# Kernel optimization log

Hardware: AMD Instinct MI355X
Metric: run time of the kernel (lower is better)

## Reference

```python
import jax, jax.numpy as jnp
import numpy as np

SCALING = 2.0  # lora alpha / r

def setup_inputs() -> dict:
    key = jax.random.key(0)
    k1, k2, k3, k4, k5 = jax.random.split(key, 5)
    B, S, D_IN, D_OUT, R = 4, 2048, 4096, 4096, 16
    x = jax.random.normal(k1, (B, S, D_IN), dtype=jnp.float32)
    weight = jax.random.normal(k2, (D_OUT, D_IN), dtype=jnp.float32) * 0.02
    lora_A = jax.random.normal(k3, (R, D_IN), dtype=jnp.float32) * (1.0 / np.sqrt(D_IN))
    lora_B = jax.random.normal(k4, (D_OUT, R), dtype=jnp.float32) * 0.02
    bias = jax.random.normal(k5, (D_OUT,), dtype=jnp.float32) * 0.02
    return {"x": x, "weight": weight, "lora_A": lora_A, "lora_B": lora_B, "bias": bias}

def reference(x, weight, lora_A, lora_B, bias):
    # Faithful to the torch module: materialize W + scaling * (B @ A), then F.linear.
    # effective_weight: [d_out, d_in]
    effective_weight = weight + SCALING * (lora_B @ lora_A)
    # F.linear(x, W, b) = x @ W.T + b
    out = jnp.einsum('bsd,od->bso', x, effective_weight) + bias
    return out
```

## Files before the change

### kernel.cpp

```cpp
#include <hip/hip_runtime.h>
#include <hip/hip_bf16.h>
#include <stdint.h>

typedef unsigned short u16;
typedef u16 u16x4 __attribute__((ext_vector_type(4)));
typedef short bf16x8 __attribute__((ext_vector_type(8)));
typedef float f32x4 __attribute__((ext_vector_type(4)));

__device__ __forceinline__ u16 f2bf(float f) {
  union { float f; uint32_t u; } v; v.f = f;
  uint32_t u = v.u;
  return (u16)((u + 0x7fffu + ((u >> 16) & 1u)) >> 16);
}

__global__ __launch_bounds__(256) void aux_kernel(
    const float4* __restrict__ x, u16x4* __restrict__ xb, int n4, int nW, int nCvt,
    const float* __restrict__ W, const float* __restrict__ A,
    const float* __restrict__ Bl, u16* __restrict__ Wout, int DIN) {
  if ((int)blockIdx.x < nW) {
    const int n0 = (int)blockIdx.x * 4;
    float bv[4][16];
#pragma unroll
    for (int j = 0; j < 4; ++j)
#pragma unroll
      for (int r = 0; r < 16; ++r) bv[j][r] = 2.0f * Bl[(n0 + j) * 16 + r];
    const int iters = DIN / (256 * 4);
    for (int c = 0; c < iters; ++c) {
      const int k = (c * 256 + (int)threadIdx.x) * 4;
      float4 wv[4];
#pragma unroll
      for (int j = 0; j < 4; ++j)
        wv[j] = *(const float4*)&W[(size_t)(n0 + j) * DIN + k];
#pragma unroll
      for (int r = 0; r < 16; ++r) {
        const float4 av = *(const float4*)&A[(size_t)r * DIN + k];
#pragma unroll
        for (int j = 0; j < 4; ++j) {
          wv[j].x += bv[j][r] * av.x;
          wv[j].y += bv[j][r] * av.y;
          wv[j].z += bv[j][r] * av.z;
          wv[j].w += bv[j][r] * av.w;
        }
      }
#pragma unroll
      for (int j = 0; j < 4; ++j) {
        u16x4 o;
        o.x = f2bf(wv[j].x); o.y = f2bf(wv[j].y);
        o.z = f2bf(wv[j].z); o.w = f2bf(wv[j].w);
        *(u16x4*)&Wout[(size_t)(n0 + j) * DIN + k] = o;
      }
    }
  } else {
    int i = ((int)blockIdx.x - nW) * 256 + threadIdx.x;
    const int stride = nCvt * 256;
    for (; i < n4; i += stride) {
      float4 v = x[i];
      u16x4 o;
      o.x = f2bf(v.x); o.y = f2bf(v.y); o.z = f2bf(v.z); o.w = f2bf(v.w);
      xb[i] = o;
    }
  }
}

#define BM 256
#define BN 256

__global__ __launch_bounds__(512, 2) void gemm256_kernel(
    const u16* __restrict__ A, const u16* __restrict__ B,
    const float* __restrict__ bias, float* __restrict__ C,
    int M, int N, int K) {
  extern __shared__ u16 lds[];

  const int tid  = threadIdx.x;
  const int lane = tid & 63;
  const int wid  = tid >> 6;

  const int nwg = gridDim.x;
  const int cpx = nwg >> 3;
  const int f   = ((int)blockIdx.x & 7) * cpx + ((int)blockIdx.x >> 3);
  const int nbx = N / BN;
  const int bx = f % nbx, by = f / nbx;
  const int bm = by * BM, bn = bx * BN;

  const int wmL = (wid >> 2) * 128;
  const int wnL = (wid & 3) * 64;
  const int lr  = lane & 15;
  const int lk  = lane >> 4;
  const int rslot = ((lk ^ ((lr >> 1) & 3)) << 3);

  const int srow  = tid >> 2;
  const int sslot = (((tid & 3) ^ ((tid >> 3) & 3)) << 3);
  const u16* gA = A + (size_t)(bm + srow) * K + sslot;
  const u16* gB = B + (size_t)(bn + srow) * K + sslot;

  auto stageA = [&](int par, int ks, int kt) {
    u16* d = &lds[(par * 2 + ks) * 8192 + wid * 512];
    const u16* s = gA + kt * 64 + ks * 32;
#pragma unroll
    for (int i = 0; i < 2; ++i)
      __builtin_amdgcn_global_load_lds(
          (__attribute__((address_space(1))) const void*)(s + (size_t)i * 128 * K),
          (__attribute__((address_space(3))) void*)(d + i * 4096), 16, 0, 0);
  };
  auto stageB = [&](int par, int ks, int kt) {
    u16* d = &lds[32768 + (par * 2 + ks) * 8192 + wid * 512];
    const u16* s = gB + kt * 64 + ks * 32;
#pragma unroll
    for (int i = 0; i < 2; ++i)
      __builtin_amdgcn_global_load_lds(
          (__attribute__((address_space(1))) const void*)(s + (size_t)i * 128 * K),
          (__attribute__((address_space(3))) void*)(d + i * 4096), 16, 0, 0);
  };

  auto ldA = [&](int par, int ks, int mf) -> bf16x8 {
    return *(const bf16x8*)&lds[(par * 2 + ks) * 8192 + (wmL + mf * 16 + lr) * 32 + rslot];
  };
  auto ldB = [&](int par, int ks, int nf) -> bf16x8 {
    return *(const bf16x8*)&lds[32768 + (par * 2 + ks) * 8192 + (wnL + nf * 16 + lr) * 32 + rslot];
  };

  f32x4 acc[8][4];
#pragma unroll
  for (int i = 0; i < 8; ++i)
#pragma unroll
    for (int n = 0; n < 4; ++n) acc[i][n] = f32x4{0.f, 0.f, 0.f, 0.f};

  const int NT = K >> 6;
  stageA(0, 0, 0); stageB(0, 0, 0); stageA(0, 1, 0); stageB(0, 1, 0);
  asm volatile("s_waitcnt vmcnt(4)" ::: "memory");
  __builtin_amdgcn_s_barrier();

  bf16x8 aE[4], aO[4], b0[4], b1[4];
#pragma unroll
  for (int n = 0; n < 4; ++n) b0[n] = ldB(0, 0, n);
#pragma unroll
  for (int m = 0; m < 4; ++m) aE[m] = ldA(0, 0, m);

#define VM4() asm volatile("s_waitcnt vmcnt(4)" ::: "memory")
#define BAR() __builtin_amdgcn_s_barrier()

  for (int t = 0; t < NT; ++t) {
    const int par = t & 1, npar = par ^ 1;
    const int tn = (t + 1 < NT) ? t + 1 : 0;

    stageA(npar, 0, tn);
#pragma unroll
    for (int m = 0; m < 4; ++m) aO[m] = ldA(par, 0, 4 + m);
    __builtin_amdgcn_s_setprio(1);
#pragma unroll
    for (int m = 0; m < 4; ++m)
#pragma unroll
      for (int n = 0; n < 4; ++n)
        acc[m][n] = __builtin_amdgcn_mfma_f32_16x16x32_bf16(aE[m], b0[n], acc[m][n], 0, 0, 0);
    __builtin_amdgcn_s_setprio(0);

    stageB(npar, 0, tn);
    VM4();
    BAR();
#pragma unroll
    for (int n = 0; n < 4; ++n) b1[n] = ldB(par, 1, n);
#pragma unroll
    for (int m = 0; m < 4; ++m) aE[m] = ldA(par, 1, m);
    __builtin_amdgcn_s_setprio(1);
#pragma unroll
    for (int m = 0; m < 4; ++m)
#pragma unroll
      for (int n = 0; n < 4; ++n)
        acc[4 + m][n] = __builtin_amdgcn_mfma_f32_16x16x32_bf16(aO[m], b0[n], acc[4 + m][n], 0, 0, 0);
    __builtin_amdgcn_s_setprio(0);

    stageA(npar, 1, tn);
#pragma unroll
    for (int m = 0; m < 4; ++m) aO[m] = ldA(par, 1, 4 + m);
    __builtin_amdgcn_s_setprio(1);
#pragma unroll
    for (int m = 0; m < 4; ++m)
#pragma unroll
      for (int n = 0; n < 4; ++n)
        acc[m][n] = __builtin_amdgcn_mfma_f32_16x16x32_bf16(aE[m], b1[n], acc[m][n], 0, 0, 0);
    __builtin_amdgcn_s_setprio(0);

    stageB(npar, 1, tn);
    VM4();
    BAR();
#pragma unroll
    for (int n = 0; n < 4; ++n) b0[n] = ldB(npar, 0, n);
#pragma unroll
    for (int m = 0; m < 4; ++m) aE[m] = ldA(npar, 0, m);
    __builtin_amdgcn_s_setprio(1);
#pragma unroll
    for (int m = 0; m < 4; ++m)
#pragma unroll
      for (int n = 0; n < 4; ++n)
        acc[4 + m][n] = __builtin_amdgcn_mfma_f32_16x16x32_bf16(aO[m], b1[n], acc[4 + m][n], 0, 0, 0);
    __builtin_amdgcn_s_setprio(0);
  }

  asm volatile("s_waitcnt vmcnt(0)" ::: "memory");
  __builtin_amdgcn_s_barrier();

#pragma unroll
  for (int nf = 0; nf < 4; ++nf) {
    const int col = bn + wnL + nf * 16 + lr;
    const float bv = bias[col];
#pragma unroll
    for (int mf = 0; mf < 8; ++mf) {
      const int row = bm + wmL + mf * 16 + lk * 4;
#pragma unroll
      for (int j = 0; j < 4; ++j)
        C[(size_t)(row + j) * N + col] = acc[mf][nf][j] + bv;
    }
  }
#undef VM4
#undef BAR
}

extern "C" void kernel_launch(void* const* d_in, const int* in_sizes, int n_in,
                              void* d_out, int out_size, void* d_ws, size_t ws_size,
                              hipStream_t stream) {
  const float* x  = (const float*)d_in[0];
  const float* w  = (const float*)d_in[1];
  const float* lA = (const float*)d_in[2];
  const float* lB = (const float*)d_in[3];
  const float* bs = (const float*)d_in[4];
  float* out = (float*)d_out;

  const int DOUT = in_sizes[4];
  const int DIN  = in_sizes[1] / DOUT;
  const int M    = in_sizes[0] / DIN;

  u16* Xb = (u16*)d_ws;
  u16* Wb = Xb + (size_t)M * DIN;

  const int n4 = (M * DIN) / 4;
  const int nW   = DOUT / 4;
  const int nCvt = 2048;
  aux_kernel<<<nW + nCvt, 256, 0, stream>>>((const float4*)x, (u16x4*)Xb, n4, nW, nCvt,
                                            w, lA, lB, Wb, DIN);

  (void)hipFuncSetAttribute((const void*)gemm256_kernel,
                            hipFuncAttributeMaxDynamicSharedMemorySize, 131072);

  const int nwg = (M / BM) * (DOUT / BN);
  gemm256_kernel<<<nwg, 512, 131072, stream>>>(Xb, Wb, bs, out, M, DOUT, DIN);
}
```

Before: 313.0 us.

## Fuse fp32-to-bf16 activation conversion into GEMM A-tile loading

Removes the separate x→bf16 conversion pass and its workspace, and has the GEMM load fp32 activations directly into registers, convert them, and write bf16 into LDS. This is meant to eliminate a full read-write round trip of the activation tensor through global memory. In exchange the A tile now streams fp32, so each GEMM block moves twice the A bytes. Register-staged loads also replace the async global-to-LDS path, which adds VGPR pressure and new waitcnt bookkeeping that could hurt overlap. Activations are reread once per N tile, so the extra fp32 traffic repeats across all column blocks.

```diff
diff --git a/kernel.cpp b/kernel.cpp
--- a/kernel.cpp
+++ b/kernel.cpp
@@ -4,6 +4,7 @@
 
 typedef unsigned short u16;
 typedef u16 u16x4 __attribute__((ext_vector_type(4)));
+typedef u16 u16x8 __attribute__((ext_vector_type(8)));
 typedef short bf16x8 __attribute__((ext_vector_type(8)));
 typedef float f32x4 __attribute__((ext_vector_type(4)));
 
@@ -13,51 +14,46 @@
   return (u16)((u + 0x7fffu + ((u >> 16) & 1u)) >> 16);
 }
 
+__device__ __forceinline__ u16x8 cvt8(f32x4 a, f32x4 b) {
+  u16x8 o;
+  o[0] = f2bf(a.x); o[1] = f2bf(a.y); o[2] = f2bf(a.z); o[3] = f2bf(a.w);
+  o[4] = f2bf(b.x); o[5] = f2bf(b.y); o[6] = f2bf(b.z); o[7] = f2bf(b.w);
+  return o;
+}
+
 __global__ __launch_bounds__(256) void aux_kernel(
-    const float4* __restrict__ x, u16x4* __restrict__ xb, int n4, int nW, int nCvt,
     const float* __restrict__ W, const float* __restrict__ A,
     const float* __restrict__ Bl, u16* __restrict__ Wout, int DIN) {
-  if ((int)blockIdx.x < nW) {
-    const int n0 = (int)blockIdx.x * 4;
-    float bv[4][16];
+  const int n0 = (int)blockIdx.x * 4;
+  float bv[4][16];
+#pragma unroll
+  for (int j = 0; j < 4; ++j)
+#pragma unroll
+    for (int r = 0; r < 16; ++r) bv[j][r] = 2.0f * Bl[(n0 + j) * 16 + r];
+  const int iters = DIN / (256 * 4);
+  for (int c = 0; c < iters; ++c) {
+    const int k = (c * 256 + (int)threadIdx.x) * 4;
+    float4 wv[4];
 #pragma unroll
     for (int j = 0; j < 4; ++j)
-#pragma unroll
-      for (int r = 0; r < 16; ++r) bv[j][r] = 2.0f * Bl[(n0 + j) * 16 + r];
-    const int iters = DIN / (256 * 4);
-    for (int c = 0; c < iters; ++c) {
-      const int k = (c * 256 + (int)threadIdx.x) * 4;
-      float4 wv[4];
-#pragma unroll
-      for (int j = 0; j < 4; ++j)
-        wv[j] = *(const float4*)&W[(size_t)(n0 + j) * DIN + k];
-#pragma unroll
-      for (int r = 0; r < 16; ++r) {
-        const float4 av = *(const float4*)&A[(size_t)r * DIN + k];
-#pragma unroll
-        for (int j = 0; j < 4; ++j) {
-          wv[j].x += bv[j][r] * av.x;
-          wv[j].y += bv[j][r] * av.y;
-          wv[j].z += bv[j][r] * av.z;
-          wv[j].w += bv[j][r] * av.w;
-        }
-      }
+      wv[j] = *(const float4*)&W[(size_t)(n0 + j) * DIN + k];
+#pragma unroll
+    for (int r = 0; r < 16; ++r) {
+      const float4 av = *(const float4*)&A[(size_t)r * DIN + k];
 #pragma unroll
       for (int j = 0; j < 4; ++j) {
-        u16x4 o;
-        o.x = f2bf(wv[j].x); o.y = f2bf(wv[j].y);
-        o.z = f2bf(wv[j].z); o.w = f2bf(wv[j].w);
-        *(u16x4*)&Wout[(size_t)(n0 + j) * DIN + k] = o;
+        wv[j].x += bv[j][r] * av.x;
+        wv[j].y += bv[j][r] * av.y;
+        wv[j].z += bv[j][r] * av.z;
+        wv[j].w += bv[j][r] * av.w;
       }
     }
-  } else {
-    int i = ((int)blockIdx.x - nW) * 256 + threadIdx.x;
-    const int stride = nCvt * 256;
-    for (; i < n4; i += stride) {
-      float4 v = x[i];
+#pragma unroll
+    for (int j = 0; j < 4; ++j) {
       u16x4 o;
-      o.x = f2bf(v.x); o.y = f2bf(v.y); o.z = f2bf(v.z); o.w = f2bf(v.w);
-      xb[i] = o;
+      o.x = f2bf(wv[j].x); o.y = f2bf(wv[j].y);
+      o.z = f2bf(wv[j].z); o.w = f2bf(wv[j].w);
+      *(u16x4*)&Wout[(size_t)(n0 + j) * DIN + k] = o;
     }
   }
 }
@@ -66,7 +62,7 @@
 #define BN 256
 
 __global__ __launch_bounds__(512, 2) void gemm256_kernel(
-    const u16* __restrict__ A, const u16* __restrict__ B,
+    const float* __restrict__ X, const u16* __restrict__ B,
     const float* __restrict__ bias, float* __restrict__ C,
     int M, int N, int K) {
   extern __shared__ u16 lds[];
@@ -90,27 +86,31 @@
 
   const int srow  = tid >> 2;
   const int sslot = (((tid & 3) ^ ((tid >> 3) & 3)) << 3);
-  const u16* gA = A + (size_t)(bm + srow) * K + sslot;
-  const u16* gB = B + (size_t)(bn + srow) * K + sslot;
-
-  auto stageA = [&](int par, int ks, int kt) {
-    u16* d = &lds[(par * 2 + ks) * 8192 + wid * 512];
-    const u16* s = gA + kt * 64 + ks * 32;
+  const float* gX = X + (size_t)(bm + srow) * K + sslot;
+  const u16*  gB = B + (size_t)(bn + srow) * K + sslot;
+
+#define PIN() asm volatile("" ::: "memory")
+
+  auto issueA = [&](int kt, int ks, f32x4* r) {
+    const float* s = gX + kt * 64 + ks * 32;
+    r[0] = *(const f32x4*)(s);
+    r[1] = *(const f32x4*)(s + 4);
+    r[2] = *(const f32x4*)(s + (size_t)128 * K);
+    r[3] = *(const f32x4*)(s + (size_t)128 * K + 4);
+  };
+  auto writeA = [&](int par, int ks, const f32x4* r) {
+    *(u16x8*)&lds[(par * 2 + ks) * 8192 + tid * 8]        = cvt8(r[0], r[1]);
+    *(u16x8*)&lds[(par * 2 + ks) * 8192 + 4096 + tid * 8] = cvt8(r[2], r[3]);
+  };
+  auto stageB = [&](int par, int ks, int kt) {
+    u16* d = &lds[32768 + (par * 2 + ks) * 8192 + wid * 512];
+    const u16* s = gB + kt * 64 + ks * 32;
 #pragma unroll
     for (int i = 0; i < 2; ++i)
       __builtin_amdgcn_global_load_lds(
           (__attribute__((address_space(1))) const void*)(s + (size_t)i * 128 * K),
           (__attribute__((address_space(3))) void*)(d + i * 4096), 16, 0, 0);
   };
-  auto stageB = [&](int par, int ks, int kt) {
-    u16* d = &lds[32768 + (par * 2 + ks) * 8192 + wid * 512];
-    const u16* s = gB + kt * 64 + ks * 32;
-#pragma unroll
-    for (int i = 0; i < 2; ++i)
-      __builtin_amdgcn_global_load_lds(
-          (__attribute__((address_space(1))) const void*)(s + (size_t)i * 128 * K),
-          (__attribute__((address_space(3))) void*)(d + i * 4096), 16, 0, 0);
-  };
 
   auto ldA = [&](int par, int ks, int mf) -> bf16x8 {
     return *(const bf16x8*)&lds[(par * 2 + ks) * 8192 + (wmL + mf * 16 + lr) * 32 + rslot];
@@ -125,25 +125,36 @@
 #pragma unroll
     for (int n = 0; n < 4; ++n) acc[i][n] = f32x4{0.f, 0.f, 0.f, 0.f};
 
+#define VM2()   asm volatile("s_waitcnt vmcnt(2)" ::: "memory")
+#define VM6()   asm volatile("s_waitcnt vmcnt(6)" ::: "memory")
+#define LGKM0() asm volatile("s_waitcnt lgkmcnt(0)" ::: "memory")
+#define BAR()   __builtin_amdgcn_s_barrier()
+
   const int NT = K >> 6;
-  stageA(0, 0, 0); stageB(0, 0, 0); stageA(0, 1, 0); stageB(0, 1, 0);
-  asm volatile("s_waitcnt vmcnt(4)" ::: "memory");
-  __builtin_amdgcn_s_barrier();
+  f32x4 rA0[4], rA1[4];
+
+  issueA(0, 0, rA0); PIN();
+  stageB(0, 0, 0);   PIN();
+  issueA(0, 1, rA1); PIN();
+  stageB(0, 1, 0);   PIN();
+  VM6();
+  writeA(0, 0, rA0);
+  LGKM0(); BAR();
 
   bf16x8 aE[4], aO[4], b0[4], b1[4];
 #pragma unroll
   for (int n = 0; n < 4; ++n) b0[n] = ldB(0, 0, n);
 #pragma unroll
   for (int m = 0; m < 4; ++m) aE[m] = ldA(0, 0, m);
-
-#define VM4() asm volatile("s_waitcnt vmcnt(4)" ::: "memory")
-#define BAR() __builtin_amdgcn_s_barrier()
 
   for (int t = 0; t < NT; ++t) {
     const int par = t & 1, npar = par ^ 1;
     const int tn = (t + 1 < NT) ? t + 1 : 0;
 
-    stageA(npar, 0, tn);
+    VM2();
+    writeA(par, 1, rA1);
+    PIN();
+    issueA(tn, 0, rA0); PIN();
 #pragma unroll
     for (int m = 0; m < 4; ++m) aO[m] = ldA(par, 0, 4 + m);
     __builtin_amdgcn_s_setprio(1);
@@ -154,8 +165,9 @@
         acc[m][n] = __builtin_amdgcn_mfma_f32_16x16x32_bf16(aE[m], b0[n], acc[m][n], 0, 0, 0);
     __builtin_amdgcn_s_setprio(0);
 
-    stageB(npar, 0, tn);
-    VM4();
+    stageB(npar, 0, tn); PIN();
+    VM6();
+    LGKM0();
     BAR();
 #pragma unroll
     for (int n = 0; n < 4; ++n) b1[n] = ldB(par, 1, n);
@@ -169,7 +181,10 @@
         acc[4 + m][n] = __builtin_amdgcn_mfma_f32_16x16x32_bf16(aO[m], b0[n], acc[4 + m][n], 0, 0, 0);
     __builtin_amdgcn_s_setprio(0);
 
-    stageA(npar, 1, tn);
+    VM2();
+    writeA(npar, 0, rA0);
+    PIN();
+    issueA(tn, 1, rA1); PIN();
 #pragma unroll
     for (int m = 0; m < 4; ++m) aO[m] = ldA(par, 1, 4 + m);
     __builtin_amdgcn_s_setprio(1);
@@ -180,8 +195,9 @@
         acc[m][n] = __builtin_amdgcn_mfma_f32_16x16x32_bf16(aE[m], b1[n], acc[m][n], 0, 0, 0);
     __builtin_amdgcn_s_setprio(0);
 
-    stageB(npar, 1, tn);
-    VM4();
+    stageB(npar, 1, tn); PIN();
+    VM6();
+    LGKM0();
     BAR();
 #pragma unroll
     for (int n = 0; n < 4; ++n) b0[n] = ldB(npar, 0, n);
@@ -211,7 +227,10 @@
         C[(size_t)(row + j) * N + col] = acc[mf][nf][j] + bv;
     }
   }
-#undef VM4
+#undef PIN
+#undef VM2
+#undef VM6
+#undef LGKM0
 #undef BAR
 }
 
@@ -229,18 +248,13 @@
   const int DIN  = in_sizes[1] / DOUT;
   const int M    = in_sizes[0] / DIN;
 
-  u16* Xb = (u16*)d_ws;
-  u16* Wb = Xb + (size_t)M * DIN;
-
-  const int n4 = (M * DIN) / 4;
-  const int nW   = DOUT / 4;
-  const int nCvt = 2048;
-  aux_kernel<<<nW + nCvt, 256, 0, stream>>>((const float4*)x, (u16x4*)Xb, n4, nW, nCvt,
-                                            w, lA, lB, Wb, DIN);
+  u16* Wb = (u16*)d_ws;
+
+  aux_kernel<<<DOUT / 4, 256, 0, stream>>>(w, lA, lB, Wb, DIN);
 
   (void)hipFuncSetAttribute((const void*)gemm256_kernel,
                             hipFuncAttributeMaxDynamicSharedMemorySize, 131072);
 
   const int nwg = (M / BM) * (DOUT / BN);
-  gemm256_kernel<<<nwg, 512, 131072, stream>>>(Xb, Wb, bs, out, M, DOUT, DIN);
-}
+  gemm256_kernel<<<nwg, 512, 131072, stream>>>(x, Wb, bs, out, M, DOUT, DIN);
+}
```

Result: slower. 337.9 us (+8.0%).
